# Kernel tuning notes

Hardware: AMD Instinct MI355X
Metric: run time of the kernel (lower is better)

The kernel has to match this reference:

```python
import jax, jax.numpy as jnp
import numpy as np

B, S, D = 2, 2048, 512
H, HD = 8, 64  # num_heads, head_size; all_head_size = H*HD = 512


def setup_inputs() -> dict:
    key = jax.random.key(0)
    ks = jax.random.split(key, 11)
    sc = 0.02
    return {
        "query": jax.random.normal(ks[0], (B, S, D), jnp.float32),
        "key": jax.random.normal(ks[1], (B, S, D), jnp.float32),
        "value": jax.random.normal(ks[2], (B, S, D), jnp.float32),
        "Wq": jax.random.normal(ks[3], (D, H * HD), jnp.float32) * sc,
        "bq": jnp.zeros((H * HD,), jnp.float32),
        "Wk": jax.random.normal(ks[4], (D, H * HD), jnp.float32) * sc,
        "bk": jnp.zeros((H * HD,), jnp.float32),
        "Wv": jax.random.normal(ks[5], (D, H * HD), jnp.float32) * sc,
        "bv": jnp.zeros((H * HD,), jnp.float32),
        "Wo": jax.random.normal(ks[6], (H * HD, D), jnp.float32) * sc,
        "bo": jnp.zeros((D,), jnp.float32),
    }


def _split_heads(x):
    b, s, _ = x.shape
    return x.reshape(b, s, H, HD).transpose(0, 2, 1, 3)  # [B,H,S,HD]


def reference(query, key, value, Wq, bq, Wk, bk, Wv, bv, Wo, bo):
    q = _split_heads(query @ Wq + bq)
    k = _split_heads(key @ Wk + bk)
    v = _split_heads(value @ Wv + bv)
    scores = jnp.einsum("bhqd,bhkd->bhqk", q, k) / jnp.sqrt(jnp.asarray(HD, q.dtype))
    probs = jax.nn.softmax(scores, axis=-1)  # dropout rate 0.0, inference
    ctx = jnp.einsum("bhqk,bhkd->bhqd", probs, v)
    ctx = ctx.transpose(0, 2, 1, 3).reshape(query.shape[0], -1, H * HD)
    return ctx @ Wo + bo
```

## Files before the change

kernel.cpp:

```cpp
#include <hip/hip_runtime.h>
#include <math.h>

#define BATCH 2
#define SEQ 2048
#define DMODEL 512
#define NH 8
#define HDIM 64
#define MTOT (BATCH * SEQ)
#define QSIZE (BATCH * NH * SEQ * HDIM)
#define WSIZE (DMODEL * DMODEL)

typedef __attribute__((ext_vector_type(8))) short bf16x8;
typedef __attribute__((ext_vector_type(4))) float f32x4;

__device__ inline unsigned short f2bf(float f) {
    union { float f; unsigned u; } v; v.f = f;
    unsigned u = v.u;
    u += 0x7fffu + ((u >> 16) & 1u);
    return (unsigned short)(u >> 16);
}
__device__ inline unsigned pack2(float lo, float hi) {
    unsigned r;
    asm("v_cvt_pk_bf16_f32 %0, %1, %2" : "=v"(r) : "v"(lo), "v"(hi));
    return r;
}

#define LSTR 72

#define WS_Q   ((size_t)0)
#define WS_K   ((size_t)QSIZE)
#define WS_V   (2 * (size_t)QSIZE)
#define WS_CTX (3 * (size_t)QSIZE)
#define WS_WT  (4 * (size_t)QSIZE)
#define WS_ABF (4 * (size_t)QSIZE + 4 * (size_t)WSIZE)

#define QSCALE 0.1803368801111204f

__global__ __launch_bounds__(256) void prep_kernel(
    const float* __restrict__ Wq, const float* __restrict__ Wk,
    const float* __restrict__ Wv, const float* __restrict__ Wo,
    const float* __restrict__ qin, const float* __restrict__ kin,
    const float* __restrict__ vin, unsigned short* __restrict__ ws)
{
    __shared__ float T[32][33];
    const int bid = blockIdx.x;
    const int tid = threadIdx.x;

    if (bid < 1024) {
        const int z = bid >> 8, rem = bid & 255;
        const float* W = (z == 0) ? Wq : (z == 1) ? Wk : (z == 2) ? Wv : Wo;
        unsigned short* Wt = ws + WS_WT + (size_t)z * WSIZE;
        const int k0 = (rem & 15) * 32, n0 = (rem >> 4) * 32;
        {
            int r = tid >> 3, c = (tid & 7) * 4;
            float4 v = *(const float4*)&W[(size_t)(k0 + r) * DMODEL + n0 + c];
            T[r][c + 0] = v.x; T[r][c + 1] = v.y; T[r][c + 2] = v.z; T[r][c + 3] = v.w;
        }
        __syncthreads();
        {
            int n = tid >> 3, c = (tid & 7) * 4;
            uint2 o;
            o.x = pack2(T[c + 0][n], T[c + 1][n]);
            o.y = pack2(T[c + 2][n], T[c + 3][n]);
            *(uint2*)&Wt[(size_t)(n0 + n) * DMODEL + k0 + c] = o;
        }
    } else {
        const int idx = bid - 1024;
        const int z = idx >> 10, blk = idx & 1023;
        const float* src = (z == 0) ? qin : (z == 1) ? kin : vin;
        unsigned short* dst = ws + WS_ABF + (size_t)z * QSIZE;
        const size_t i = ((size_t)blk * 256 + tid) * 8;
        float4 f0 = *(const float4*)(src + i);
        float4 f1 = *(const float4*)(src + i + 4);
        uint4 o;
        o.x = pack2(f0.x, f0.y); o.y = pack2(f0.z, f0.w);
        o.z = pack2(f1.x, f1.y); o.w = pack2(f1.z, f1.w);
        *(uint4*)(dst + i) = o;
    }
}

__global__ __launch_bounds__(256) void qkv_mfma_kernel(
    unsigned short* __restrict__ ws,
    const float* __restrict__ bq, const float* __restrict__ bk,
    const float* __restrict__ bv)
{
    const int which = blockIdx.z;
    const unsigned short* A  = ws + WS_ABF + (size_t)which * QSIZE;
    const unsigned short* Wt = ws + WS_WT + (size_t)which * WSIZE;
    const float* bias = (which == 0) ? bq : (which == 1) ? bk : bv;
    unsigned short* out = ws + (size_t)which * QSIZE;

    __shared__ __align__(16) short As[128][LSTR];
    __shared__ __align__(16) short Bs[128][LSTR];

    const int tid = threadIdx.x;
    const int lane = tid & 63, wave = tid >> 6;
    const int lrow = lane & 15, quad = lane >> 4;
    const int m0 = blockIdx.y * 128, n0 = blockIdx.x * 128;

    const int sr = tid >> 1;
    const int sh = (tid & 1) * 32;
    const unsigned short* ap0 = A  + (size_t)(m0 + sr) * DMODEL + sh;
    const unsigned short* wp0 = Wt + (size_t)(n0 + sr) * DMODEL + sh;

    f32x4 acc[2][8];
    #pragma unroll
    for (int i = 0; i < 2; ++i)
        #pragma unroll
        for (int n = 0; n < 8; ++n) acc[i][n] = f32x4{0.f, 0.f, 0.f, 0.f};

    uint4 a0, a1, a2, a3, b0, b1, b2, b3;
#define LOADS(K0) do { \
        const unsigned short* ap = ap0 + (K0); \
        const unsigned short* wp = wp0 + (K0); \
        a0 = *(const uint4*)(ap + 0);  a1 = *(const uint4*)(ap + 8); \
        a2 = *(const uint4*)(ap + 16); a3 = *(const uint4*)(ap + 24); \
        b0 = *(const uint4*)(wp + 0);  b1 = *(const uint4*)(wp + 8); \
        b2 = *(const uint4*)(wp + 16); b3 = *(const uint4*)(wp + 24); } while (0)
#define WRITES() do { \
        *(uint4*)&As[sr][sh + 0]  = a0; *(uint4*)&As[sr][sh + 8]  = a1; \
        *(uint4*)&As[sr][sh + 16] = a2; *(uint4*)&As[sr][sh + 24] = a3; \
        *(uint4*)&Bs[sr][sh + 0]  = b0; *(uint4*)&Bs[sr][sh + 8]  = b1; \
        *(uint4*)&Bs[sr][sh + 16] = b2; *(uint4*)&Bs[sr][sh + 24] = b3; } while (0)

    LOADS(0);

    #pragma unroll
    for (int kk = 0; kk < 8; ++kk) {
        const int k0 = kk * 64;
        __syncthreads();
        WRITES();
        __syncthreads();
        if (kk < 7) LOADS(k0 + 64);
        __builtin_amdgcn_s_setprio(1);
        #pragma unroll
        for (int s = 0; s < 2; ++s) {
            bf16x8 af[2];
            #pragma unroll
            for (int i = 0; i < 2; ++i)
                af[i] = *(const bf16x8*)&As[wave * 32 + i * 16 + lrow][s * 32 + quad * 8];
            #pragma unroll
            for (int n = 0; n < 8; ++n) {
                bf16x8 bfv = *(const bf16x8*)&Bs[n * 16 + lrow][s * 32 + quad * 8];
                acc[0][n] = __builtin_amdgcn_mfma_f32_16x16x32_bf16(af[0], bfv, acc[0][n], 0, 0, 0);
                acc[1][n] = __builtin_amdgcn_mfma_f32_16x16x32_bf16(af[1], bfv, acc[1][n], 0, 0, 0);
            }
        }
        __builtin_amdgcn_s_setprio(0);
    }
#undef LOADS
#undef WRITES

    if (which < 2) {
        const float scale = (which == 0) ? QSCALE : 1.0f;
        #pragma unroll
        for (int n = 0; n < 8; ++n) {
            const int col = n0 + n * 16 + lrow;
            const int h_ = col >> 6, hd_ = col & 63;
            const float bv_ = bias[col];
            #pragma unroll
            for (int i = 0; i < 2; ++i) {
                #pragma unroll
                for (int r = 0; r < 4; ++r) {
                    const int m = m0 + wave * 32 + i * 16 + quad * 4 + r;
                    const int b_ = m >> 11, s_ = m & (SEQ - 1);
                    const float v = (acc[i][n][r] + bv_) * scale;
                    out[((size_t)((b_ * NH + h_) * SEQ + s_)) * HDIM + hd_] = f2bf(v);
                }
            }
        }
    } else {
        #pragma unroll
        for (int n = 0; n < 8; ++n) {
            const int col = n0 + n * 16 + lrow;
            const int h_ = col >> 6, hd_ = col & 63;
            const float bv_ = bias[col];
            #pragma unroll
            for (int i = 0; i < 2; ++i) {
                const int m = m0 + wave * 32 + i * 16 + quad * 4;
                const int b_ = m >> 11, s_ = m & (SEQ - 1);
                uint2 o;
                o.x = pack2(acc[i][n][0] + bv_, acc[i][n][1] + bv_);
                o.y = pack2(acc[i][n][2] + bv_, acc[i][n][3] + bv_);
                *(uint2*)&out[((size_t)((b_ * NH + h_) * HDIM + hd_)) * SEQ + s_] = o;
            }
        }
    }
}

#define HSEQ (SEQ / 2)
#define NT   (HSEQ / 64)
#define OSTR 68
#define THR2 11.0f

__global__ __launch_bounds__(512) void attn_mfma_kernel(
    const unsigned short* __restrict__ ws, unsigned short* __restrict__ ctx)
{
    const unsigned short* Q = ws + WS_Q;
    const unsigned short* K = ws + WS_K;
    const unsigned short* V = ws + WS_V;

    __shared__ __align__(16) short Ks[2][2][64][LSTR];
    __shared__ __align__(16) short Vt[2][2][64][LSTR];

    const int lin = blockIdx.x + 16 * blockIdx.y;
    const int bh  = (lin & 7) + 8 * (lin >> 8);
    const int q0  = ((lin >> 3) & 31) * 64;

    const int tid = threadIdx.x;
    const int lane = tid & 63, wave = tid >> 6;
    const int half = wave >> 2, w4 = wave & 3;
    const int lrow = lane & 15, quad = lane >> 4;
    const size_t base = (size_t)bh * SEQ * HDIM;

    const unsigned short* qrow = Q + base + (size_t)(q0 + w4 * 16 + lrow) * HDIM;
    const bf16x8 qb0 = *(const bf16x8*)(qrow + quad * 8);
    const bf16x8 qb1 = *(const bf16x8*)(qrow + 32 + quad * 8);

    float m_prev = -1e30f, l_run = 0.f;
    f32x4 oacc[4];
    #pragma unroll
    for (int n = 0; n < 4; ++n) oacc[n] = f32x4{0.f, 0.f, 0.f, 0.f};

    const int t  = tid & 255;
    const int kr = t >> 2;
    const int kc = (t & 3) * 16;
    const int n_ = t & 3;
    const int c0 = ((n_ >= 2) ? 32 : 0) + (n_ & 1) * 4;
    const int ktbase = half * HSEQ;

    const unsigned short* kptr = K + base + (size_t)(ktbase + kr) * HDIM + kc;
    const unsigned short* vptr = V + base + (size_t)kr * SEQ + ktbase + kc;

    uint4 kA, kB, vA, vB;
#define LOADT(TI) do { \
        const unsigned short* kp = kptr + (size_t)(TI) * 64 * HDIM; \
        const unsigned short* vp = vptr + (TI) * 64; \
        kA = *(const uint4*)kp; kB = *(const uint4*)(kp + 8); \
        vA = *(const uint4*)vp; vB = *(const uint4*)(vp + 8); \
    } while (0)
#define WRITET(BUF) do { \
        *(uint4*)&Ks[half][BUF][kr][kc]     = kA; \
        *(uint4*)&Ks[half][BUF][kr][kc + 8] = kB; \
        uint2 w0; w0.x = vA.x; w0.y = vA.y; \
        uint2 w1; w1.x = vA.z; w1.y = vA.w; \
        uint2 w2; w2.x = vB.x; w2.y = vB.y; \
        uint2 w3; w3.x = vB.z; w3.y = vB.w; \
        *(uint2*)&Vt[half][BUF][kr][c0]      = w0; \
        *(uint2*)&Vt[half][BUF][kr][c0 + 8]  = w1; \
        *(uint2*)&Vt[half][BUF][kr][c0 + 16] = w2; \
        *(uint2*)&Vt[half][BUF][kr][c0 + 24] = w3; \
    } while (0)

    LOADT(0);
    WRITET(0);
    LOADT(1);

    #pragma unroll 2
    for (int ti = 0; ti < NT; ++ti) {
        const int cur = ti & 1;
        __syncthreads();

        f32x4 st[4];
        __builtin_amdgcn_s_setprio(1);
        #pragma unroll
        for (int n = 0; n < 4; ++n) {
            bf16x8 ka0 = *(const bf16x8*)&Ks[half][cur][n * 16 + lrow][quad * 8];
            bf16x8 ka1 = *(const bf16x8*)&Ks[half][cur][n * 16 + lrow][32 + quad * 8];
            f32x4 z = f32x4{0.f, 0.f, 0.f, 0.f};
            z = __builtin_amdgcn_mfma_f32_16x16x32_bf16(ka0, qb0, z, 0, 0, 0);
            z = __builtin_amdgcn_mfma_f32_16x16x32_bf16(ka1, qb1, z, 0, 0, 0);
            st[n] = z;
        }
        __builtin_amdgcn_s_setprio(0);

        float t0 = fmaxf(fmaxf(st[0][0], st[0][1]), fmaxf(st[0][2], st[0][3]));
        float t1 = fmaxf(fmaxf(st[1][0], st[1][1]), fmaxf(st[1][2], st[1][3]));
        float t2 = fmaxf(fmaxf(st[2][0], st[2][1]), fmaxf(st[2][2], st[2][3]));
        float t3 = fmaxf(fmaxf(st[3][0], st[3][1]), fmaxf(st[3][2], st[3][3]));
        float tmax = fmaxf(fmaxf(t0, t1), fmaxf(t2, t3));
        tmax = fmaxf(tmax, __shfl_xor(tmax, 16));
        tmax = fmaxf(tmax, __shfl_xor(tmax, 32));

        if (!__all(tmax <= m_prev + THR2)) {
            const float mnew = fmaxf(m_prev, tmax);
            const float alpha = exp2f(m_prev - mnew);
            l_run *= alpha;
            #pragma unroll
            for (int n = 0; n < 4; ++n) {
                oacc[n][0] *= alpha; oacc[n][1] *= alpha;
                oacc[n][2] *= alpha; oacc[n][3] *= alpha;
            }
            m_prev = mnew;
        }

        float p[4][4];
        float tsum = 0.f;
        #pragma unroll
        for (int n = 0; n < 4; ++n)
            #pragma unroll
            for (int r = 0; r < 4; ++r) {
                p[n][r] = exp2f(st[n][r] - m_prev);
                tsum += p[n][r];
            }
        l_run += tsum;

        union { unsigned w[4]; bf16x8 v; } U0, U1;
        U0.w[0] = pack2(p[0][0], p[0][1]); U0.w[1] = pack2(p[0][2], p[0][3]);
        U0.w[2] = pack2(p[1][0], p[1][1]); U0.w[3] = pack2(p[1][2], p[1][3]);
        U1.w[0] = pack2(p[2][0], p[2][1]); U1.w[1] = pack2(p[2][2], p[2][3]);
        U1.w[2] = pack2(p[3][0], p[3][1]); U1.w[3] = pack2(p[3][2], p[3][3]);

        __builtin_amdgcn_s_setprio(1);
        #pragma unroll
        for (int n = 0; n < 4; ++n) {
            bf16x8 va0 = *(const bf16x8*)&Vt[half][cur][n * 16 + lrow][quad * 8];
            bf16x8 va1 = *(const bf16x8*)&Vt[half][cur][n * 16 + lrow][32 + quad * 8];
            oacc[n] = __builtin_amdgcn_mfma_f32_16x16x32_bf16(va0, U0.v, oacc[n], 0, 0, 0);
            oacc[n] = __builtin_amdgcn_mfma_f32_16x16x32_bf16(va1, U1.v, oacc[n], 0, 0, 0);
        }
        __builtin_amdgcn_s_setprio(0);

        if (ti < NT - 1) WRITET(cur ^ 1);
        if (ti < NT - 2) LOADT(ti + 2);
    }
#undef LOADT
#undef WRITET

    l_run += __shfl_xor(l_run, 16);
    l_run += __shfl_xor(l_run, 32);

    __syncthreads();
    float* Obuf = (float*)&Ks[0][0][0][0];
    float* Mbuf = (float*)&Vt[0][0][0][0];

    if (half == 1) {
        float* ob = Obuf + (size_t)w4 * (16 * OSTR) + (size_t)lrow * OSTR;
        #pragma unroll
        for (int n = 0; n < 4; ++n)
            *(f32x4*)&ob[n * 16 + quad * 4] = oacc[n];
        if (quad == 0) {
            Mbuf[w4 * 16 + lrow]      = m_prev;
            Mbuf[64 + w4 * 16 + lrow] = l_run;
        }
    }
    __syncthreads();
    if (half == 0) {
        const float m1 = Mbuf[w4 * 16 + lrow];
        const float l1 = Mbuf[64 + w4 * 16 + lrow];
        const float M  = fmaxf(m_prev, m1);
        const float a0 = exp2f(m_prev - M), a1 = exp2f(m1 - M);
        const float inv = 1.f / (l_run * a0 + l1 * a1);
        const float s0 = a0 * inv, s1 = a1 * inv;
        const float* ob = Obuf + (size_t)w4 * (16 * OSTR) + (size_t)lrow * OSTR;

        const int b_ = bh >> 3, h_ = bh & 7;
        const int qg = q0 + w4 * 16 + lrow;
        unsigned short* crow = ctx + ((size_t)(b_ * SEQ + qg)) * DMODEL + h_ * HDIM;
        #pragma unroll
        for (int n = 0; n < 4; ++n) {
            f32x4 o1 = *(const f32x4*)&ob[n * 16 + quad * 4];
            uint2 o;
            o.x = pack2(oacc[n][0] * s0 + o1[0] * s1, oacc[n][1] * s0 + o1[1] * s1);
            o.y = pack2(oacc[n][2] * s0 + o1[2] * s1, oacc[n][3] * s0 + o1[3] * s1);
            *(uint2*)&crow[n * 16 + quad * 4] = o;
        }
    }
}

__global__ __launch_bounds__(256) void out_proj_mfma_kernel(
    const unsigned short* __restrict__ ws, const float* __restrict__ bo,
    float* __restrict__ out)
{
    const unsigned short* ctx = ws + WS_CTX;
    const unsigned short* Wt  = ws + WS_WT + 3 * (size_t)WSIZE;

    __shared__ __align__(16) short As[128][LSTR];
    __shared__ __align__(16) short Bs[64][LSTR];

    const int tid = threadIdx.x;
    const int lane = tid & 63, wave = tid >> 6;
    const int lrow = lane & 15, quad = lane >> 4;
    const int m0 = blockIdx.y * 128, n0 = blockIdx.x * 64;

    const int sr = tid >> 1, sh = (tid & 1) * 32;
    const int br = tid >> 2, bqr = (tid & 3) * 16;
    const unsigned short* ap0 = ctx + (size_t)(m0 + sr) * DMODEL + sh;
    const unsigned short* wp0 = Wt + (size_t)(n0 + br) * DMODEL + bqr;

    f32x4 acc[2][4];
    #pragma unroll
    for (int i = 0; i < 2; ++i)
        #pragma unroll
        for (int n = 0; n < 4; ++n) acc[i][n] = f32x4{0.f, 0.f, 0.f, 0.f};

    uint4 a0, a1, a2, a3, b0, b1;
#define LOADS(K0) do { \
        const unsigned short* ap = ap0 + (K0); \
        const unsigned short* wp = wp0 + (K0); \
        a0 = *(const uint4*)(ap + 0);  a1 = *(const uint4*)(ap + 8); \
        a2 = *(const uint4*)(ap + 16); a3 = *(const uint4*)(ap + 24); \
        b0 = *(const uint4*)wp; b1 = *(const uint4*)(wp + 8); } while (0)
#define WRITES() do { \
        *(uint4*)&As[sr][sh + 0]  = a0; *(uint4*)&As[sr][sh + 8]  = a1; \
        *(uint4*)&As[sr][sh + 16] = a2; *(uint4*)&As[sr][sh + 24] = a3; \
        *(uint4*)&Bs[br][bqr]     = b0; *(uint4*)&Bs[br][bqr + 8] = b1; } while (0)

    LOADS(0);

    #pragma unroll
    for (int kk = 0; kk < 8; ++kk) {
        const int k0 = kk * 64;
        __syncthreads();
        WRITES();
        __syncthreads();
        if (kk < 7) LOADS(k0 + 64);
        __builtin_amdgcn_s_setprio(1);
        #pragma unroll
        for (int s = 0; s < 2; ++s) {
            bf16x8 af[2];
            #pragma unroll
            for (int i = 0; i < 2; ++i)
                af[i] = *(const bf16x8*)&As[wave * 32 + i * 16 + lrow][s * 32 + quad * 8];
            #pragma unroll
            for (int n = 0; n < 4; ++n) {
                bf16x8 bfv = *(const bf16x8*)&Bs[n * 16 + lrow][s * 32 + quad * 8];
                acc[0][n] = __builtin_amdgcn_mfma_f32_16x16x32_bf16(af[0], bfv, acc[0][n], 0, 0, 0);
                acc[1][n] = __builtin_amdgcn_mfma_f32_16x16x32_bf16(af[1], bfv, acc[1][n], 0, 0, 0);
            }
        }
        __builtin_amdgcn_s_setprio(0);
    }
#undef LOADS
#undef WRITES

    #pragma unroll
    for (int n = 0; n < 4; ++n) {
        const int col = n0 + n * 16 + lrow;
        const float bv_ = bo[col];
        #pragma unroll
        for (int i = 0; i < 2; ++i) {
            #pragma unroll
            for (int r = 0; r < 4; ++r) {
                const int m = m0 + wave * 32 + i * 16 + quad * 4 + r;
                out[(size_t)m * DMODEL + col] = acc[i][n][r] + bv_;
            }
        }
    }
}

extern "C" void kernel_launch(void* const* d_in, const int* in_sizes, int n_in,
                              void* d_out, int out_size, void* d_ws, size_t ws_size,
                              hipStream_t stream)
{
    const float* qin = (const float*)d_in[0];
    const float* kin = (const float*)d_in[1];
    const float* vin = (const float*)d_in[2];
    const float* Wq  = (const float*)d_in[3];
    const float* bq  = (const float*)d_in[4];
    const float* Wk  = (const float*)d_in[5];
    const float* bk  = (const float*)d_in[6];
    const float* Wv  = (const float*)d_in[7];
    const float* bv  = (const float*)d_in[8];
    const float* Wo  = (const float*)d_in[9];
    const float* bo  = (const float*)d_in[10];

    unsigned short* ws = (unsigned short*)d_ws;
    float* out = (float*)d_out;

    prep_kernel<<<4096, 256, 0, stream>>>(Wq, Wk, Wv, Wo, qin, kin, vin, ws);

    dim3 gp(DMODEL / 128, MTOT / 128, 3);
    qkv_mfma_kernel<<<gp, 256, 0, stream>>>(ws, bq, bk, bv);

    dim3 ga(BATCH * NH, SEQ / 64);
    attn_mfma_kernel<<<ga, 512, 0, stream>>>(ws, ws + WS_CTX);

    dim3 go(DMODEL / 64, MTOT / 128);
    out_proj_mfma_kernel<<<go, 256, 0, stream>>>(ws, bo, out);
}
```

Before: 148.7 us.

## Fuse fp32-to-bf16 activation conversion into QKV GEMM and stage V transpose via LDS

The separate pass in prep_kernel that converted the query, key and value activations to bf16 is removed. The QKV GEMM now loads fp32 activations directly and packs them to bf16 while writing shared memory, which saves a full write and re-read of three bf16 activation buffers. The transposed V output is also staged through shared memory so each thread writes contiguous 16-byte chunks along the sequence dimension instead of scattered 8-byte stores. The cost is twice the global read bytes for the A operand inside the GEMM, more live registers per thread, and extra barriers in the V epilogue.

```diff
diff --git a/kernel.cpp b/kernel.cpp
--- a/kernel.cpp
+++ b/kernel.cpp
@@ -26,72 +26,60 @@
 }
 
 #define LSTR 72
+#define VSTR 136
 
 #define WS_Q   ((size_t)0)
 #define WS_K   ((size_t)QSIZE)
 #define WS_V   (2 * (size_t)QSIZE)
 #define WS_CTX (3 * (size_t)QSIZE)
 #define WS_WT  (4 * (size_t)QSIZE)
-#define WS_ABF (4 * (size_t)QSIZE + 4 * (size_t)WSIZE)
 
 #define QSCALE 0.1803368801111204f
 
 __global__ __launch_bounds__(256) void prep_kernel(
     const float* __restrict__ Wq, const float* __restrict__ Wk,
     const float* __restrict__ Wv, const float* __restrict__ Wo,
-    const float* __restrict__ qin, const float* __restrict__ kin,
-    const float* __restrict__ vin, unsigned short* __restrict__ ws)
+    unsigned short* __restrict__ ws)
 {
     __shared__ float T[32][33];
     const int bid = blockIdx.x;
     const int tid = threadIdx.x;
 
-    if (bid < 1024) {
-        const int z = bid >> 8, rem = bid & 255;
-        const float* W = (z == 0) ? Wq : (z == 1) ? Wk : (z == 2) ? Wv : Wo;
-        unsigned short* Wt = ws + WS_WT + (size_t)z * WSIZE;
-        const int k0 = (rem & 15) * 32, n0 = (rem >> 4) * 32;
-        {
-            int r = tid >> 3, c = (tid & 7) * 4;
-            float4 v = *(const float4*)&W[(size_t)(k0 + r) * DMODEL + n0 + c];
-            T[r][c + 0] = v.x; T[r][c + 1] = v.y; T[r][c + 2] = v.z; T[r][c + 3] = v.w;
-        }
-        __syncthreads();
-        {
-            int n = tid >> 3, c = (tid & 7) * 4;
-            uint2 o;
-            o.x = pack2(T[c + 0][n], T[c + 1][n]);
-            o.y = pack2(T[c + 2][n], T[c + 3][n]);
-            *(uint2*)&Wt[(size_t)(n0 + n) * DMODEL + k0 + c] = o;
-        }
-    } else {
-        const int idx = bid - 1024;
-        const int z = idx >> 10, blk = idx & 1023;
-        const float* src = (z == 0) ? qin : (z == 1) ? kin : vin;
-        unsigned short* dst = ws + WS_ABF + (size_t)z * QSIZE;
-        const size_t i = ((size_t)blk * 256 + tid) * 8;
-        float4 f0 = *(const float4*)(src + i);
-        float4 f1 = *(const float4*)(src + i + 4);
-        uint4 o;
-        o.x = pack2(f0.x, f0.y); o.y = pack2(f0.z, f0.w);
-        o.z = pack2(f1.x, f1.y); o.w = pack2(f1.z, f1.w);
-        *(uint4*)(dst + i) = o;
+    const int z = bid >> 8, rem = bid & 255;
+    const float* W = (z == 0) ? Wq : (z == 1) ? Wk : (z == 2) ? Wv : Wo;
+    unsigned short* Wt = ws + WS_WT + (size_t)z * WSIZE;
+    const int k0 = (rem & 15) * 32, n0 = (rem >> 4) * 32;
+    {
+        int r = tid >> 3, c = (tid & 7) * 4;
+        float4 v = *(const float4*)&W[(size_t)(k0 + r) * DMODEL + n0 + c];
+        T[r][c + 0] = v.x; T[r][c + 1] = v.y; T[r][c + 2] = v.z; T[r][c + 3] = v.w;
+    }
+    __syncthreads();
+    {
+        int n = tid >> 3, c = (tid & 7) * 4;
+        uint2 o;
+        o.x = pack2(T[c + 0][n], T[c + 1][n]);
+        o.y = pack2(T[c + 2][n], T[c + 3][n]);
+        *(uint2*)&Wt[(size_t)(n0 + n) * DMODEL + k0 + c] = o;
     }
 }
 
 __global__ __launch_bounds__(256) void qkv_mfma_kernel(
     unsigned short* __restrict__ ws,
+    const float* __restrict__ qin, const float* __restrict__ kin,
+    const float* __restrict__ vin,
     const float* __restrict__ bq, const float* __restrict__ bk,
     const float* __restrict__ bv)
 {
     const int which = blockIdx.z;
-    const unsigned short* A  = ws + WS_ABF + (size_t)which * QSIZE;
+    const float* A = (which == 0) ? qin : (which == 1) ? kin : vin;
     const unsigned short* Wt = ws + WS_WT + (size_t)which * WSIZE;
     const float* bias = (which == 0) ? bq : (which == 1) ? bk : bv;
     unsigned short* out = ws + (size_t)which * QSIZE;
 
-    __shared__ __align__(16) short As[128][LSTR];
-    __shared__ __align__(16) short Bs[128][LSTR];
+    __shared__ __align__(16) short SMEM[2][128][LSTR];
+    auto As = SMEM[0];
+    auto Bs = SMEM[1];
 
     const int tid = threadIdx.x;
     const int lane = tid & 63, wave = tid >> 6;
@@ -100,7 +88,7 @@
 
     const int sr = tid >> 1;
     const int sh = (tid & 1) * 32;
-    const unsigned short* ap0 = A  + (size_t)(m0 + sr) * DMODEL + sh;
+    const float*          ap0 = A  + (size_t)(m0 + sr) * DMODEL + sh;
     const unsigned short* wp0 = Wt + (size_t)(n0 + sr) * DMODEL + sh;
 
     f32x4 acc[2][8];
@@ -109,17 +97,31 @@
         #pragma unroll
         for (int n = 0; n < 8; ++n) acc[i][n] = f32x4{0.f, 0.f, 0.f, 0.f};
 
-    uint4 a0, a1, a2, a3, b0, b1, b2, b3;
+    float4 fa0, fa1, fa2, fa3, fa4, fa5, fa6, fa7;
+    uint4 b0, b1, b2, b3;
 #define LOADS(K0) do { \
-        const unsigned short* ap = ap0 + (K0); \
+        const float* ap = ap0 + (K0); \
         const unsigned short* wp = wp0 + (K0); \
-        a0 = *(const uint4*)(ap + 0);  a1 = *(const uint4*)(ap + 8); \
-        a2 = *(const uint4*)(ap + 16); a3 = *(const uint4*)(ap + 24); \
+        fa0 = *(const float4*)(ap + 0);  fa1 = *(const float4*)(ap + 4); \
+        fa2 = *(const float4*)(ap + 8);  fa3 = *(const float4*)(ap + 12); \
+        fa4 = *(const float4*)(ap + 16); fa5 = *(const float4*)(ap + 20); \
+        fa6 = *(const float4*)(ap + 24); fa7 = *(const float4*)(ap + 28); \
         b0 = *(const uint4*)(wp + 0);  b1 = *(const uint4*)(wp + 8); \
         b2 = *(const uint4*)(wp + 16); b3 = *(const uint4*)(wp + 24); } while (0)
 #define WRITES() do { \
-        *(uint4*)&As[sr][sh + 0]  = a0; *(uint4*)&As[sr][sh + 8]  = a1; \
-        *(uint4*)&As[sr][sh + 16] = a2; *(uint4*)&As[sr][sh + 24] = a3; \
+        uint4 u; \
+        u.x = pack2(fa0.x, fa0.y); u.y = pack2(fa0.z, fa0.w); \
+        u.z = pack2(fa1.x, fa1.y); u.w = pack2(fa1.z, fa1.w); \
+        *(uint4*)&As[sr][sh + 0] = u; \
+        u.x = pack2(fa2.x, fa2.y); u.y = pack2(fa2.z, fa2.w); \
+        u.z = pack2(fa3.x, fa3.y); u.w = pack2(fa3.z, fa3.w); \
+        *(uint4*)&As[sr][sh + 8] = u; \
+        u.x = pack2(fa4.x, fa4.y); u.y = pack2(fa4.z, fa4.w); \
+        u.z = pack2(fa5.x, fa5.y); u.w = pack2(fa5.z, fa5.w); \
+        *(uint4*)&As[sr][sh + 16] = u; \
+        u.x = pack2(fa6.x, fa6.y); u.y = pack2(fa6.z, fa6.w); \
+        u.z = pack2(fa7.x, fa7.y); u.w = pack2(fa7.z, fa7.w); \
+        *(uint4*)&As[sr][sh + 24] = u; \
         *(uint4*)&Bs[sr][sh + 0]  = b0; *(uint4*)&Bs[sr][sh + 8]  = b1; \
         *(uint4*)&Bs[sr][sh + 16] = b2; *(uint4*)&Bs[sr][sh + 24] = b3; } while (0)
 
@@ -170,21 +172,30 @@
             }
         }
     } else {
+        __syncthreads();
+        short* Vl = &SMEM[0][0][0];
         #pragma unroll
         for (int n = 0; n < 8; ++n) {
-            const int col = n0 + n * 16 + lrow;
-            const int h_ = col >> 6, hd_ = col & 63;
-            const float bv_ = bias[col];
+            const int colp = n * 16 + lrow;
+            const float bv_ = bias[n0 + colp];
             #pragma unroll
             for (int i = 0; i < 2; ++i) {
-                const int m = m0 + wave * 32 + i * 16 + quad * 4;
-                const int b_ = m >> 11, s_ = m & (SEQ - 1);
                 uint2 o;
                 o.x = pack2(acc[i][n][0] + bv_, acc[i][n][1] + bv_);
                 o.y = pack2(acc[i][n][2] + bv_, acc[i][n][3] + bv_);
-                *(uint2*)&out[((size_t)((b_ * NH + h_) * HDIM + hd_)) * SEQ + s_] = o;
-            }
-        }
+                *(uint2*)&Vl[colp * VSTR + wave * 32 + i * 16 + quad * 4] = o;
+            }
+        }
+        __syncthreads();
+        const int row = tid >> 1, halfc = tid & 1;
+        const int gcol = n0 + row, h_ = gcol >> 6, hd_ = gcol & 63;
+        const int b_ = m0 >> 11;
+        const int s0_ = (m0 & (SEQ - 1)) + halfc * 64;
+        unsigned short* dst = out + ((size_t)((b_ * NH + h_) * HDIM + hd_)) * SEQ + s0_;
+        const short* src = &Vl[row * VSTR + halfc * 64];
+        #pragma unroll
+        for (int j = 0; j < 8; ++j)
+            *(uint4*)(dst + j * 8) = *(const uint4*)(src + j * 8);
     }
 }
 
@@ -468,10 +479,10 @@
     unsigned short* ws = (unsigned short*)d_ws;
     float* out = (float*)d_out;
 
-    prep_kernel<<<4096, 256, 0, stream>>>(Wq, Wk, Wv, Wo, qin, kin, vin, ws);
+    prep_kernel<<<1024, 256, 0, stream>>>(Wq, Wk, Wv, Wo, ws);
 
     dim3 gp(DMODEL / 128, MTOT / 128, 3);
-    qkv_mfma_kernel<<<gp, 256, 0, stream>>>(ws, bq, bk, bv);
+    qkv_mfma_kernel<<<gp, 256, 0, stream>>>(ws, qin, kin, vin, bq, bk, bv);
 
     dim3 ga(BATCH * NH, SEQ / 64);
     attn_mfma_kernel<<<ga, 512, 0, stream>>>(ws, ws + WS_CTX);
```

New measurement: 156.1 us. +4.9%, slower.
